# Optimization experiments

Hardware: AMD Instinct MI355X
Metric: run time of the kernel (lower is better)

## Reference

```python
import jax, jax.numpy as jnp
import numpy as np

H = 12        # num_attention_heads
D = 768       # hidden_size
DH = D // H   # attention_size per head (64)
B, S = 1, 4096


def setup_inputs() -> dict:
    key = jax.random.key(0)
    ks = jax.random.split(key, 10)
    scale = 0.02
    x = jax.random.normal(ks[0], (B, S, D), dtype=jnp.float32)
    # per-head QKV weights stacked: [H, D, DH]
    wq = jax.random.normal(ks[1], (H, D, DH), dtype=jnp.float32) * scale
    wk = jax.random.normal(ks[2], (H, D, DH), dtype=jnp.float32) * scale
    wv = jax.random.normal(ks[3], (H, D, DH), dtype=jnp.float32) * scale
    bq = jax.random.normal(ks[4], (H, DH), dtype=jnp.float32) * scale
    bk = jax.random.normal(ks[5], (H, DH), dtype=jnp.float32) * scale
    bv = jax.random.normal(ks[6], (H, DH), dtype=jnp.float32) * scale
    wo = jax.random.normal(ks[7], (D, D), dtype=jnp.float32) * scale
    bo = jax.random.normal(ks[8], (D,), dtype=jnp.float32) * scale
    return {"x": x, "wq": wq, "bq": bq, "wk": wk, "bk": bk,
            "wv": wv, "bv": bv, "wo": wo, "bo": bo}


def reference(x, wq, bq, wk, bk, wv, bv, wo, bo):
    # per-head linear projections: [B,S,D] x [H,D,DH] -> [B,H,S,DH]
    q = jnp.einsum('bsd,hde->bhse', x, wq) + bq[None, :, None, :]
    k = jnp.einsum('bsd,hde->bhse', x, wk) + bk[None, :, None, :]
    v = jnp.einsum('bsd,hde->bhse', x, wv) + bv[None, :, None, :]
    # scaled dot-product attention, full NxN probs as in original
    scores = jnp.einsum('bhse,bhte->bhst', q, k) / jnp.sqrt(jnp.float32(DH))
    probs = jax.nn.softmax(scores, axis=-1)          # [B,H,S,S]
    ctx = jnp.einsum('bhst,bhte->bhse', probs, v)    # [B,H,S,DH]
    # concat heads along feature dim (head order = original ModuleList order)
    ctx = jnp.transpose(ctx, (0, 2, 1, 3)).reshape(B, S, H * DH)
    out = ctx @ wo + bo                               # output projection
    return out
```

## Files before the change

kernel.cpp:

```cpp
#include <hip/hip_runtime.h>


using frag8 = __attribute__((ext_vector_type(8))) short;
using facc4 = __attribute__((ext_vector_type(4))) float;
using uint4v = __attribute__((ext_vector_type(4))) unsigned int;

#define LOG2E 1.4426950408889634f
#define SWZ16(r, b) ((b) ^ (((r) & 7) << 4))

#if defined(__has_builtin)
#  if __has_builtin(__builtin_amdgcn_exp2f)
#    define EXP2(x) __builtin_amdgcn_exp2f(x)
#  else
#    define EXP2(x) exp2f(x)
#  endif
#else
#  define EXP2(x) exp2f(x)
#endif

__device__ __forceinline__ unsigned short f2bf(float f) {
  unsigned int u = __builtin_bit_cast(unsigned int, f);
  u = (u + 0x7FFFu + ((u >> 16) & 1u)) >> 16;
  return (unsigned short)u;
}
__device__ __forceinline__ float bf2f(unsigned short s) {
  unsigned int u = ((unsigned int)s) << 16;
  return __builtin_bit_cast(float, u);
}
__device__ __forceinline__ unsigned cvt_pk_bf16(float lo, float hi) {
  unsigned r;
  asm("v_cvt_pk_bf16_f32 %0, %1, %2" : "=v"(r) : "v"(lo), "v"(hi));
  return r;
}

__device__ __forceinline__ facc4 mfma_bf16(frag8 a, frag8 b, facc4 c) {
  return __builtin_amdgcn_mfma_f32_16x16x32_bf16(a, b, c, 0, 0, 0);
}

__device__ __forceinline__ void gld_lds16(const void* g, void* l) {
  auto gp = (const __attribute__((address_space(1))) unsigned int*)g;
  auto lp = (__attribute__((address_space(3))) unsigned int*)l;
  __builtin_amdgcn_global_load_lds(gp, lp, 16, 0, 0);
}

__global__ __launch_bounds__(256) void k_cvt_x(const float* __restrict__ in,
                                               unsigned short* __restrict__ out) {
  int i = (blockIdx.x * 256 + threadIdx.x) * 8;
  float4 a = *(const float4*)(in + i);
  float4 b = *(const float4*)(in + i + 4);
  frag8 r;
  r[0] = (short)f2bf(a.x); r[1] = (short)f2bf(a.y);
  r[2] = (short)f2bf(a.z); r[3] = (short)f2bf(a.w);
  r[4] = (short)f2bf(b.x); r[5] = (short)f2bf(b.y);
  r[6] = (short)f2bf(b.z); r[7] = (short)f2bf(b.w);
  *(frag8*)(out + i) = r;
}

__global__ __launch_bounds__(256) void k_prep_w(
    const float* __restrict__ wq, const float* __restrict__ wk,
    const float* __restrict__ wv, const float* __restrict__ wo,
    unsigned short* __restrict__ wqT, unsigned short* __restrict__ wkT,
    unsigned short* __restrict__ wvT, unsigned short* __restrict__ woT) {
  __shared__ unsigned short tile[64][65];
  const int bx = blockIdx.x;
  const float* src; unsigned short* dst;
  int ld_src, ld_dst, r0, c0;
  if (bx < 432) {
    int p = bx / 144, rem = bx % 144;
    int h = rem / 12, dt = rem % 12;
    src = (p == 0 ? wq : (p == 1 ? wk : wv)) + (size_t)h * 768 * 64;
    dst = (p == 0 ? wqT : (p == 1 ? wkT : wvT)) + (size_t)h * 64 * 768;
    ld_src = 64; ld_dst = 768; r0 = dt * 64; c0 = 0;
  } else {
    int t = bx - 432;
    src = wo; dst = woT;
    ld_src = 768; ld_dst = 768;
    r0 = (t / 12) * 64; c0 = (t % 12) * 64;
  }
  const int tid = threadIdx.x;
  const int lr = tid >> 2, lc0 = (tid & 3) * 16;
#pragma unroll
  for (int i = 0; i < 16; ++i)
    tile[lr][lc0 + i] = f2bf(src[(size_t)(r0 + lr) * ld_src + c0 + lc0 + i]);
  __syncthreads();
  const int oc = tid >> 2;
#pragma unroll
  for (int i = 0; i < 16; ++i)
    dst[(size_t)(c0 + oc) * ld_dst + r0 + lc0 + i] = tile[lc0 + i][oc];
}

__global__ __launch_bounds__(256) void k_qkv(
    const unsigned short* __restrict__ xb, const unsigned short* __restrict__ wT,
    const float* __restrict__ bq, const float* __restrict__ bk,
    const float* __restrict__ bv,
    unsigned short* __restrict__ qo, unsigned short* __restrict__ ko,
    unsigned short* __restrict__ vTo) {
  __shared__ __align__(16) unsigned short As[128 * 64];
  __shared__ __align__(16) unsigned short Bs[64 * 64];
  const int sb = blockIdx.x, ph = blockIdx.y;
  const int p = ph / 12, h = ph % 12;
  const int s0 = sb * 128;
  const int tid = threadIdx.x;
  const int w = tid >> 6, l = tid & 63;
  const int lg = l >> 4, li = l & 15;
  const int wm = w >> 1, wn = w & 1;
  const unsigned short* wTb = wT + (size_t)ph * 64 * 768;

  facc4 acc[4][2];
#pragma unroll
  for (int i = 0; i < 4; ++i)
#pragma unroll
    for (int j = 0; j < 2; ++j) acc[i][j] = (facc4){0.f, 0.f, 0.f, 0.f};

  const int rA = tid >> 3;
  const int cbp = (tid & 7) * 16;

  for (int k0 = 0; k0 < 768; k0 += 64) {
#pragma unroll
    for (int i = 0; i < 4; ++i) {
      int r = i * 32 + rA;
      gld_lds16((const char*)(xb + (size_t)(s0 + r) * 768 + k0) + SWZ16(r, cbp),
                (char*)As + i * 4096 + w * 1024);
    }
#pragma unroll
    for (int i = 0; i < 2; ++i) {
      int r = i * 32 + rA;
      gld_lds16((const char*)(wTb + (size_t)r * 768 + k0) + SWZ16(r, cbp),
                (char*)Bs + i * 4096 + w * 1024);
    }
    __syncthreads();
#pragma unroll
    for (int kk = 0; kk < 2; ++kk) {
      const int cbl = kk * 64 + lg * 16;
      frag8 a[4], b[2];
#pragma unroll
      for (int mf = 0; mf < 4; ++mf) {
        int r = wm * 64 + mf * 16 + li;
        a[mf] = *(const frag8*)((const char*)As + r * 128 + SWZ16(r, cbl));
      }
#pragma unroll
      for (int nf = 0; nf < 2; ++nf) {
        int r = wn * 32 + nf * 16 + li;
        b[nf] = *(const frag8*)((const char*)Bs + r * 128 + SWZ16(r, cbl));
      }
#pragma unroll
      for (int mf = 0; mf < 4; ++mf)
#pragma unroll
        for (int nf = 0; nf < 2; ++nf)
          acc[mf][nf] = mfma_bf16(a[mf], b[nf], acc[mf][nf]);
    }
    __syncthreads();
  }

  const float* bias = (p == 0 ? bq : (p == 1 ? bk : bv)) + h * 64;
  const float scale = (p == 0) ? 0.125f * LOG2E : 1.0f;
  float bvv[2];
#pragma unroll
  for (int nf = 0; nf < 2; ++nf) bvv[nf] = bias[wn * 32 + nf * 16 + li];
#pragma unroll
  for (int mf = 0; mf < 4; ++mf)
#pragma unroll
    for (int nf = 0; nf < 2; ++nf) {
      int e = wn * 32 + nf * 16 + li;
#pragma unroll
      for (int j = 0; j < 4; ++j) {
        int s = s0 + wm * 64 + mf * 16 + lg * 4 + j;
        unsigned short bf = f2bf((acc[mf][nf][j] + bvv[nf]) * scale);
        if (p == 0)      qo[((size_t)h * 4096 + s) * 64 + e] = bf;
        else if (p == 1) ko[((size_t)h * 4096 + s) * 64 + e] = bf;
        else             vTo[((size_t)h * 64 + e) * 4096 + s] = bf;
      }
    }
}

__global__ __launch_bounds__(512) void k_attn(
    const unsigned short* __restrict__ q, const unsigned short* __restrict__ k,
    const unsigned short* __restrict__ vT,
    unsigned short* __restrict__ oP, float* __restrict__ lP) {
  __shared__ __align__(16) char Kb[2][8192];
  __shared__ __align__(16) char Vb[2][8192];
  const int bid = blockIdx.x;
  const int part = blockIdx.y;
  const int h = bid >> 5, qb = bid & 31;
  const int s0 = qb * 128;
  const int tid = threadIdx.x;
  const int w = tid >> 6, l = tid & 63;
  const int lg = l >> 4, li = l & 15;
  const unsigned short* Kh = k + (size_t)h * 4096 * 64;
  const unsigned short* Vh = vT + (size_t)h * 64 * 4096;

  const int rS = tid >> 3;
  const int bS = (tid & 7) * 16;
  const int sbS = SWZ16(rS, bS);

  const unsigned short* qrow = q + ((size_t)h * 4096 + s0 + w * 16 + li) * 64;
  frag8 qf0 = *(const frag8*)(qrow + lg * 8);
  frag8 qf1 = *(const frag8*)(qrow + 32 + lg * 8);

  frag8 onesf;
#pragma unroll
  for (int i = 0; i < 8; ++i) onesf[i] = (short)0x3F80;

  const int a_ = li >> 2, b_ = li & 3;
  const int r_base = 8 * a_ + b_;
  int kOff[4][2], vOff[4][2];
#pragma unroll
  for (int cn = 0; cn < 4; ++cn) {
    int r = r_base + 4 * ((cn & 1) ^ (a_ & 1)) + 32 * (cn >> 1);
    kOff[cn][0] = r * 128 + SWZ16(r, lg * 16);
    kOff[cn][1] = r * 128 + SWZ16(r, 64 + lg * 16);
  }
#pragma unroll
  for (int nf = 0; nf < 4; ++nf) {
    int rv = nf * 16 + li;
    vOff[nf][0] = rv * 128 + SWZ16(rv, lg * 16);
    vOff[nf][1] = rv * 128 + SWZ16(rv, 64 + lg * 16);
  }
  const char* KbC = (const char*)Kb;
  const char* VbC = (const char*)Vb;

  facc4 acc[4];
  facc4 accl = (facc4){0.f, 0.f, 0.f, 0.f};
#pragma unroll
  for (int nf = 0; nf < 4; ++nf) acc[nf] = (facc4){0.f, 0.f, 0.f, 0.f};

  const int kb0 = part * 2048;

  gld_lds16((const char*)(Kh + (size_t)(kb0 + rS) * 64) + sbS, (char*)Kb + w * 1024);
  gld_lds16((const char*)(Vh + (size_t)rS * 4096 + kb0) + sbS, (char*)Vb + w * 1024);
  const char* KgN = (const char*)(Kh + (size_t)(kb0 + 64 + rS) * 64) + sbS;
  const char* VgN = (const char*)(Vh + (size_t)rS * 4096 + kb0 + 64) + sbS;
  __syncthreads();

#define ATTN_STEP(BUFB, KT)                                                   \
  {                                                                           \
    if ((KT) < 31) {                                                          \
      gld_lds16(KgN, (char*)Kb + ((BUFB) ^ 8192) + w * 1024);                 \
      gld_lds16(VgN, (char*)Vb + ((BUFB) ^ 8192) + w * 1024);                 \
      KgN += 8192; VgN += 128;                                                \
    }                                                                         \
    facc4 sf[4];                                                              \
    __builtin_amdgcn_s_setprio(1);                                            \
    _Pragma("unroll")                                                         \
    for (int cn = 0; cn < 4; ++cn) {                                          \
      frag8 a0 = *(const frag8*)(KbC + (BUFB) + kOff[cn][0]);                 \
      frag8 a1 = *(const frag8*)(KbC + (BUFB) + kOff[cn][1]);                 \
      facc4 s = (facc4){0.f, 0.f, 0.f, 0.f};                                  \
      s = mfma_bf16(a0, qf0, s);                                              \
      s = mfma_bf16(a1, qf1, s);                                              \
      sf[cn] = s;                                                             \
    }                                                                         \
    __builtin_amdgcn_s_setprio(0);                                            \
    if (lg & 1) {                                                             \
      facc4 t_ = sf[0]; sf[0] = sf[1]; sf[1] = t_;                            \
      t_ = sf[2]; sf[2] = sf[3]; sf[3] = t_;                                  \
    }                                                                         \
    uint4v u0, u1;                                                            \
    u0[0] = cvt_pk_bf16(EXP2(sf[0][0]), EXP2(sf[0][1]));                      \
    u0[1] = cvt_pk_bf16(EXP2(sf[0][2]), EXP2(sf[0][3]));                      \
    u0[2] = cvt_pk_bf16(EXP2(sf[1][0]), EXP2(sf[1][1]));                      \
    u0[3] = cvt_pk_bf16(EXP2(sf[1][2]), EXP2(sf[1][3]));                      \
    u1[0] = cvt_pk_bf16(EXP2(sf[2][0]), EXP2(sf[2][1]));                      \
    u1[1] = cvt_pk_bf16(EXP2(sf[2][2]), EXP2(sf[2][3]));                      \
    u1[2] = cvt_pk_bf16(EXP2(sf[3][0]), EXP2(sf[3][1]));                      \
    u1[3] = cvt_pk_bf16(EXP2(sf[3][2]), EXP2(sf[3][3]));                      \
    frag8 pa0 = __builtin_bit_cast(frag8, u0);                                \
    frag8 pa1 = __builtin_bit_cast(frag8, u1);                                \
    __builtin_amdgcn_s_setprio(1);                                            \
    accl = mfma_bf16(pa0, onesf, accl);                                       \
    accl = mfma_bf16(pa1, onesf, accl);                                       \
    _Pragma("unroll")                                                         \
    for (int nf = 0; nf < 4; ++nf) {                                          \
      frag8 vb0 = *(const frag8*)(VbC + (BUFB) + vOff[nf][0]);                \
      frag8 vb1 = *(const frag8*)(VbC + (BUFB) + vOff[nf][1]);                \
      acc[nf] = mfma_bf16(pa0, vb0, acc[nf]);                                 \
      acc[nf] = mfma_bf16(pa1, vb1, acc[nf]);                                 \
    }                                                                         \
    __builtin_amdgcn_s_setprio(0);                                            \
    __syncthreads();                                                          \
  }

  for (int t2 = 0; t2 < 16; ++t2) {
    ATTN_STEP(0, 2 * t2)
    ATTN_STEP(8192, 2 * t2 + 1)
  }
#undef ATTN_STEP

  const size_t base = ((size_t)(part * 12 + h) * 4096 + s0 + w * 16);
#pragma unroll
  for (int nf = 0; nf < 4; ++nf)
#pragma unroll
    for (int j = 0; j < 4; ++j)
      oP[(base + lg * 4 + j) * 64 + nf * 16 + li] = f2bf(acc[nf][j] / accl[j]);
  if (li == 0) {
#pragma unroll
    for (int j = 0; j < 4; ++j)
      lP[base + lg * 4 + j] = accl[j];
  }
}

__global__ __launch_bounds__(256) void k_proj(
    const unsigned short* __restrict__ oP, const float* __restrict__ lP,
    const unsigned short* __restrict__ woT, const float* __restrict__ bo,
    float* __restrict__ out) {
  __shared__ __align__(16) unsigned short As[64 * 64];
  __shared__ __align__(16) unsigned short Bs[64 * 64];
  const int s0 = blockIdx.x * 64, j0 = blockIdx.y * 64;
  const int tid = threadIdx.x;
  const int w = tid >> 6, l = tid & 63;
  const int lg = l >> 4, li = l & 15;
  const int wm = w >> 1, wn = w & 1;
  facc4 acc[2][2];
#pragma unroll
  for (int i = 0; i < 2; ++i)
#pragma unroll
    for (int j = 0; j < 2; ++j) acc[i][j] = (facc4){0.f, 0.f, 0.f, 0.f};

  const int rA = tid >> 3;
  const int c8 = (tid & 7) * 8;
  const int cbp = c8 * 2;

  for (int k0 = 0; k0 < 768; k0 += 64) {
    const int hh = k0 >> 6;
#pragma unroll
    for (int i = 0; i < 2; ++i) {
      int r = i * 32 + rA;
      gld_lds16((const char*)(woT + (size_t)(j0 + r) * 768 + k0) + SWZ16(r, cbp),
                (char*)Bs + i * 4096 + w * 1024);
    }
#pragma unroll
    for (int i = 0; i < 2; ++i) {
      int r = i * 32 + rA;
      int s = s0 + r;
      size_t r0 = (size_t)hh * 4096 + s;
      size_t r1 = (size_t)(12 + hh) * 4096 + s;
      frag8 o0 = *(const frag8*)(oP + r0 * 64 + c8);
      frag8 o1 = *(const frag8*)(oP + r1 * 64 + c8);
      float l0 = lP[r0], l1 = lP[r1];
      float inv = 1.f / (l0 + l1);
      float w0 = l0 * inv, w1 = l1 * inv;
      frag8 cv;
#pragma unroll
      for (int t = 0; t < 8; ++t)
        cv[t] = (short)f2bf(w0 * bf2f((unsigned short)o0[t]) +
                            w1 * bf2f((unsigned short)o1[t]));
      *(frag8*)((char*)As + r * 128 + SWZ16(r, cbp)) = cv;
    }
    __syncthreads();
#pragma unroll
    for (int kk = 0; kk < 2; ++kk) {
      const int cbl = kk * 64 + lg * 16;
      frag8 a[2], b[2];
#pragma unroll
      for (int mf = 0; mf < 2; ++mf) {
        int r = wm * 32 + mf * 16 + li;
        a[mf] = *(const frag8*)((const char*)As + r * 128 + SWZ16(r, cbl));
      }
#pragma unroll
      for (int nf = 0; nf < 2; ++nf) {
        int r = wn * 32 + nf * 16 + li;
        b[nf] = *(const frag8*)((const char*)Bs + r * 128 + SWZ16(r, cbl));
      }
#pragma unroll
      for (int mf = 0; mf < 2; ++mf)
#pragma unroll
        for (int nf = 0; nf < 2; ++nf)
          acc[mf][nf] = mfma_bf16(a[mf], b[nf], acc[mf][nf]);
    }
    __syncthreads();
  }
#pragma unroll
  for (int nf = 0; nf < 2; ++nf) {
    int jc = j0 + wn * 32 + nf * 16 + li;
    float bb = bo[jc];
#pragma unroll
    for (int mf = 0; mf < 2; ++mf)
#pragma unroll
      for (int j = 0; j < 4; ++j) {
        int s = s0 + wm * 32 + mf * 16 + lg * 4 + j;
        out[(size_t)s * 768 + jc] = acc[mf][nf][j] + bb;
      }
  }
}

extern "C" void kernel_launch(void* const* d_in, const int* in_sizes, int n_in,
                              void* d_out, int out_size, void* d_ws, size_t ws_size,
                              hipStream_t stream) {
  const float* x  = (const float*)d_in[0];
  const float* wq = (const float*)d_in[1];
  const float* bq = (const float*)d_in[2];
  const float* wk = (const float*)d_in[3];
  const float* bk = (const float*)d_in[4];
  const float* wv = (const float*)d_in[5];
  const float* bv = (const float*)d_in[6];
  const float* wo = (const float*)d_in[7];
  const float* bo = (const float*)d_in[8];
  float* out = (float*)d_out;

  char* ws = (char*)d_ws;
  unsigned short* xb  = (unsigned short*)(ws);
  unsigned short* wT  = (unsigned short*)(ws + 6291456);
  unsigned short* woT = (unsigned short*)(ws + 9830400);
  unsigned short* qd  = (unsigned short*)(ws + 11010048);
  unsigned short* kd  = (unsigned short*)(ws + 17301504);
  unsigned short* vTd = (unsigned short*)(ws + 23592960);
  unsigned short* oP  = (unsigned short*)(ws + 36175872);
  float*          lP  = (float*)(ws + 48758784);

  k_cvt_x<<<1536, 256, 0, stream>>>(x, xb);
  k_prep_w<<<576, 256, 0, stream>>>(wq, wk, wv, wo,
                                    wT, wT + 589824, wT + 1179648, woT);
  k_qkv<<<dim3(32, 36), 256, 0, stream>>>(xb, wT, bq, bk, bv, qd, kd, vTd);
  k_attn<<<dim3(384, 2), 512, 0, stream>>>(qd, kd, vTd, oP, lP);
  k_proj<<<dim3(64, 12), 256, 0, stream>>>(oP, lP, woT, bo, out);
}
```

Before: 122.7 us.

## Process two 16-row query tiles per wave in attention to reuse K/V fragments

The attention kernel now runs 4 waves per block (256 threads) instead of 8, and each wave handles two 16-row query sub-tiles (A and B, 64 rows apart). Each K and V fragment read from LDS feeds twice as many MFMAs. Each thread issues two async loads per tile instead of one to keep the shared-memory fill the same. This roughly doubles accumulator and score registers per wave and halves the waves per block, which may hurt latency hiding.

```diff
diff --git a/kernel.cpp b/kernel.cpp
--- a/kernel.cpp
+++ b/kernel.cpp
@@ -173,7 +173,7 @@
     }
 }
 
-__global__ __launch_bounds__(512) void k_attn(
+__global__ __launch_bounds__(256) void k_attn(
     const unsigned short* __restrict__ q, const unsigned short* __restrict__ k,
     const unsigned short* __restrict__ vT,
     unsigned short* __restrict__ oP, float* __restrict__ lP) {
@@ -193,9 +193,12 @@
   const int bS = (tid & 7) * 16;
   const int sbS = SWZ16(rS, bS);
 
-  const unsigned short* qrow = q + ((size_t)h * 4096 + s0 + w * 16 + li) * 64;
-  frag8 qf0 = *(const frag8*)(qrow + lg * 8);
-  frag8 qf1 = *(const frag8*)(qrow + 32 + lg * 8);
+  const unsigned short* qrowA = q + ((size_t)h * 4096 + s0 + w * 16 + li) * 64;
+  const unsigned short* qrowB = qrowA + (size_t)64 * 64;
+  frag8 qfA0 = *(const frag8*)(qrowA + lg * 8);
+  frag8 qfA1 = *(const frag8*)(qrowA + 32 + lg * 8);
+  frag8 qfB0 = *(const frag8*)(qrowB + lg * 8);
+  frag8 qfB1 = *(const frag8*)(qrowB + 32 + lg * 8);
 
   frag8 onesf;
 #pragma unroll
@@ -219,62 +222,96 @@
   const char* KbC = (const char*)Kb;
   const char* VbC = (const char*)Vb;
 
-  facc4 acc[4];
-  facc4 accl = (facc4){0.f, 0.f, 0.f, 0.f};
-#pragma unroll
-  for (int nf = 0; nf < 4; ++nf) acc[nf] = (facc4){0.f, 0.f, 0.f, 0.f};
+  facc4 accA[4], accB[4];
+  facc4 acclA = (facc4){0.f, 0.f, 0.f, 0.f};
+  facc4 acclB = (facc4){0.f, 0.f, 0.f, 0.f};
+#pragma unroll
+  for (int nf = 0; nf < 4; ++nf) {
+    accA[nf] = (facc4){0.f, 0.f, 0.f, 0.f};
+    accB[nf] = (facc4){0.f, 0.f, 0.f, 0.f};
+  }
 
   const int kb0 = part * 2048;
 
-  gld_lds16((const char*)(Kh + (size_t)(kb0 + rS) * 64) + sbS, (char*)Kb + w * 1024);
-  gld_lds16((const char*)(Vh + (size_t)rS * 4096 + kb0) + sbS, (char*)Vb + w * 1024);
-  const char* KgN = (const char*)(Kh + (size_t)(kb0 + 64 + rS) * 64) + sbS;
-  const char* VgN = (const char*)(Vh + (size_t)rS * 4096 + kb0 + 64) + sbS;
+  gld_lds16((const char*)(Kh + (size_t)(kb0 + rS) * 64) + sbS,
+            (char*)Kb + w * 1024);
+  gld_lds16((const char*)(Kh + (size_t)(kb0 + 32 + rS) * 64) + sbS,
+            (char*)Kb + 4096 + w * 1024);
+  gld_lds16((const char*)(Vh + (size_t)rS * 4096 + kb0) + sbS,
+            (char*)Vb + w * 1024);
+  gld_lds16((const char*)(Vh + (size_t)(rS + 32) * 4096 + kb0) + sbS,
+            (char*)Vb + 4096 + w * 1024);
+  const char* Kg0 = (const char*)(Kh + (size_t)(kb0 + 64 + rS) * 64) + sbS;
+  const char* Kg1 = (const char*)(Kh + (size_t)(kb0 + 96 + rS) * 64) + sbS;
+  const char* Vg0 = (const char*)(Vh + (size_t)rS * 4096 + kb0 + 64) + sbS;
+  const char* Vg1 = (const char*)(Vh + (size_t)(rS + 32) * 4096 + kb0 + 64) + sbS;
   __syncthreads();
 
 #define ATTN_STEP(BUFB, KT)                                                   \
   {                                                                           \
     if ((KT) < 31) {                                                          \
-      gld_lds16(KgN, (char*)Kb + ((BUFB) ^ 8192) + w * 1024);                 \
-      gld_lds16(VgN, (char*)Vb + ((BUFB) ^ 8192) + w * 1024);                 \
-      KgN += 8192; VgN += 128;                                                \
+      gld_lds16(Kg0, (char*)Kb + ((BUFB) ^ 8192) + w * 1024);                 \
+      gld_lds16(Kg1, (char*)Kb + ((BUFB) ^ 8192) + 4096 + w * 1024);          \
+      gld_lds16(Vg0, (char*)Vb + ((BUFB) ^ 8192) + w * 1024);                 \
+      gld_lds16(Vg1, (char*)Vb + ((BUFB) ^ 8192) + 4096 + w * 1024);          \
+      Kg0 += 8192; Kg1 += 8192; Vg0 += 128; Vg1 += 128;                       \
     }                                                                         \
-    facc4 sf[4];                                                              \
+    facc4 sfA[4], sfB[4];                                                     \
     __builtin_amdgcn_s_setprio(1);                                            \
     _Pragma("unroll")                                                         \
     for (int cn = 0; cn < 4; ++cn) {                                          \
       frag8 a0 = *(const frag8*)(KbC + (BUFB) + kOff[cn][0]);                 \
       frag8 a1 = *(const frag8*)(KbC + (BUFB) + kOff[cn][1]);                 \
-      facc4 s = (facc4){0.f, 0.f, 0.f, 0.f};                                  \
-      s = mfma_bf16(a0, qf0, s);                                              \
-      s = mfma_bf16(a1, qf1, s);                                              \
-      sf[cn] = s;                                                             \
+      facc4 sA = (facc4){0.f, 0.f, 0.f, 0.f};                                 \
+      facc4 sB = (facc4){0.f, 0.f, 0.f, 0.f};                                 \
+      sA = mfma_bf16(a0, qfA0, sA);                                           \
+      sA = mfma_bf16(a1, qfA1, sA);                                           \
+      sB = mfma_bf16(a0, qfB0, sB);                                           \
+      sB = mfma_bf16(a1, qfB1, sB);                                           \
+      sfA[cn] = sA; sfB[cn] = sB;                                             \
     }                                                                         \
     __builtin_amdgcn_s_setprio(0);                                            \
     if (lg & 1) {                                                             \
-      facc4 t_ = sf[0]; sf[0] = sf[1]; sf[1] = t_;                            \
-      t_ = sf[2]; sf[2] = sf[3]; sf[3] = t_;                                  \
+      facc4 t_;                                                               \
+      t_ = sfA[0]; sfA[0] = sfA[1]; sfA[1] = t_;                              \
+      t_ = sfA[2]; sfA[2] = sfA[3]; sfA[3] = t_;                              \
+      t_ = sfB[0]; sfB[0] = sfB[1]; sfB[1] = t_;                              \
+      t_ = sfB[2]; sfB[2] = sfB[3]; sfB[3] = t_;                              \
     }                                                                         \
-    uint4v u0, u1;                                                            \
-    u0[0] = cvt_pk_bf16(EXP2(sf[0][0]), EXP2(sf[0][1]));                      \
-    u0[1] = cvt_pk_bf16(EXP2(sf[0][2]), EXP2(sf[0][3]));                      \
-    u0[2] = cvt_pk_bf16(EXP2(sf[1][0]), EXP2(sf[1][1]));                      \
-    u0[3] = cvt_pk_bf16(EXP2(sf[1][2]), EXP2(sf[1][3]));                      \
-    u1[0] = cvt_pk_bf16(EXP2(sf[2][0]), EXP2(sf[2][1]));                      \
-    u1[1] = cvt_pk_bf16(EXP2(sf[2][2]), EXP2(sf[2][3]));                      \
-    u1[2] = cvt_pk_bf16(EXP2(sf[3][0]), EXP2(sf[3][1]));                      \
-    u1[3] = cvt_pk_bf16(EXP2(sf[3][2]), EXP2(sf[3][3]));                      \
-    frag8 pa0 = __builtin_bit_cast(frag8, u0);                                \
-    frag8 pa1 = __builtin_bit_cast(frag8, u1);                                \
+    uint4v uA0, uA1, uB0, uB1;                                                \
+    uA0[0] = cvt_pk_bf16(EXP2(sfA[0][0]), EXP2(sfA[0][1]));                   \
+    uA0[1] = cvt_pk_bf16(EXP2(sfA[0][2]), EXP2(sfA[0][3]));                   \
+    uA0[2] = cvt_pk_bf16(EXP2(sfA[1][0]), EXP2(sfA[1][1]));                   \
+    uA0[3] = cvt_pk_bf16(EXP2(sfA[1][2]), EXP2(sfA[1][3]));                   \
+    uA1[0] = cvt_pk_bf16(EXP2(sfA[2][0]), EXP2(sfA[2][1]));                   \
+    uA1[1] = cvt_pk_bf16(EXP2(sfA[2][2]), EXP2(sfA[2][3]));                   \
+    uA1[2] = cvt_pk_bf16(EXP2(sfA[3][0]), EXP2(sfA[3][1]));                   \
+    uA1[3] = cvt_pk_bf16(EXP2(sfA[3][2]), EXP2(sfA[3][3]));                   \
+    uB0[0] = cvt_pk_bf16(EXP2(sfB[0][0]), EXP2(sfB[0][1]));                   \
+    uB0[1] = cvt_pk_bf16(EXP2(sfB[0][2]), EXP2(sfB[0][3]));                   \
+    uB0[2] = cvt_pk_bf16(EXP2(sfB[1][0]), EXP2(sfB[1][1]));                   \
+    uB0[3] = cvt_pk_bf16(EXP2(sfB[1][2]), EXP2(sfB[1][3]));                   \
+    uB1[0] = cvt_pk_bf16(EXP2(sfB[2][0]), EXP2(sfB[2][1]));                   \
+    uB1[1] = cvt_pk_bf16(EXP2(sfB[2][2]), EXP2(sfB[2][3]));                   \
+    uB1[2] = cvt_pk_bf16(EXP2(sfB[3][0]), EXP2(sfB[3][1]));                   \
+    uB1[3] = cvt_pk_bf16(EXP2(sfB[3][2]), EXP2(sfB[3][3]));                   \
+    frag8 paA0 = __builtin_bit_cast(frag8, uA0);                              \
+    frag8 paA1 = __builtin_bit_cast(frag8, uA1);                              \
+    frag8 paB0 = __builtin_bit_cast(frag8, uB0);                              \
+    frag8 paB1 = __builtin_bit_cast(frag8, uB1);                              \
     __builtin_amdgcn_s_setprio(1);                                            \
-    accl = mfma_bf16(pa0, onesf, accl);                                       \
-    accl = mfma_bf16(pa1, onesf, accl);                                       \
+    acclA = mfma_bf16(paA0, onesf, acclA);                                    \
+    acclA = mfma_bf16(paA1, onesf, acclA);                                    \
+    acclB = mfma_bf16(paB0, onesf, acclB);                                    \
+    acclB = mfma_bf16(paB1, onesf, acclB);                                    \
     _Pragma("unroll")                                                         \
     for (int nf = 0; nf < 4; ++nf) {                                          \
       frag8 vb0 = *(const frag8*)(VbC + (BUFB) + vOff[nf][0]);                \
       frag8 vb1 = *(const frag8*)(VbC + (BUFB) + vOff[nf][1]);                \
-      acc[nf] = mfma_bf16(pa0, vb0, acc[nf]);                                 \
-      acc[nf] = mfma_bf16(pa1, vb1, acc[nf]);                                 \
+      accA[nf] = mfma_bf16(paA0, vb0, accA[nf]);                              \
+      accA[nf] = mfma_bf16(paA1, vb1, accA[nf]);                              \
+      accB[nf] = mfma_bf16(paB0, vb0, accB[nf]);                              \
+      accB[nf] = mfma_bf16(paB1, vb1, accB[nf]);                              \
     }                                                                         \
     __builtin_amdgcn_s_setprio(0);                                            \
     __syncthreads();                                                          \
@@ -286,16 +323,21 @@
   }
 #undef ATTN_STEP
 
-  const size_t base = ((size_t)(part * 12 + h) * 4096 + s0 + w * 16);
+  const size_t baseA = ((size_t)(part * 12 + h) * 4096 + s0 + w * 16);
+  const size_t baseB = baseA + 64;
 #pragma unroll
   for (int nf = 0; nf < 4; ++nf)
 #pragma unroll
-    for (int j = 0; j < 4; ++j)
-      oP[(base + lg * 4 + j) * 64 + nf * 16 + li] = f2bf(acc[nf][j] / accl[j]);
+    for (int j = 0; j < 4; ++j) {
+      oP[(baseA + lg * 4 + j) * 64 + nf * 16 + li] = f2bf(accA[nf][j] / acclA[j]);
+      oP[(baseB + lg * 4 + j) * 64 + nf * 16 + li] = f2bf(accB[nf][j] / acclB[j]);
+    }
   if (li == 0) {
 #pragma unroll
-    for (int j = 0; j < 4; ++j)
-      lP[base + lg * 4 + j] = accl[j];
+    for (int j = 0; j < 4; ++j) {
+      lP[baseA + lg * 4 + j] = acclA[j];
+      lP[baseB + lg * 4 + j] = acclB[j];
+    }
   }
 }
 
@@ -411,6 +453,6 @@
   k_prep_w<<<576, 256, 0, stream>>>(wq, wk, wv, wo,
                                     wT, wT + 589824, wT + 1179648, woT);
   k_qkv<<<dim3(32, 36), 256, 0, stream>>>(xb, wT, bq, bk, bv, qd, kd, vTd);
-  k_attn<<<dim3(384, 2), 512, 0, stream>>>(qd, kd, vTd, oP, lP);
+  k_attn<<<dim3(384, 2), 256, 0, stream>>>(qd, kd, vTd, oP, lP);
   k_proj<<<dim3(64, 12), 256, 0, stream>>>(oP, lP, woT, bo, out);
 }
```

Result: slower. 136.3 us (+11.1%).
